# Kernel tuning notes

Hardware: AMD Instinct MI355X
Metric: run time of the kernel (lower is better)

## Reference

```python
import jax, jax.numpy as jnp
import numpy as np
import math

HID = 128
NH = 8
HD = HID // NH
NL = 3
CLIP = 10.0
EPS = 1e-5

def _ln(x, g, b):
    mu = jnp.mean(x, axis=-1, keepdims=True)
    var = jnp.var(x, axis=-1, keepdims=True)
    return (x - mu) * jax.lax.rsqrt(var + EPS) * g + b

def _layer(h, e_bias1, e_gate2, g1, b1, wh, g2, b2, w1, w2):
    B, N, _ = h.shape
    h_in = h
    hn = _ln(h, g1, b1)
    qkv = hn @ wh                                   # (B,N,3H)
    q, k, v = jnp.split(qkv, 3, axis=-1)
    q = q.reshape(B, N, NH, HD).transpose(0, 2, 1, 3)  # (B,nh,N,hd)
    k = k.reshape(B, N, NH, HD).transpose(0, 2, 1, 3)
    v = v.reshape(B, N, NH, HD).transpose(0, 2, 1, 3)
    att = jnp.einsum('bhid,bhjd->bhij', q, k) * (1.0 / math.sqrt(HD))
    att = jax.nn.softmax(att + e_bias1, axis=-1) * e_gate2
    y = jnp.einsum('bhij,bhjd->bhid', att, v)
    y = y.transpose(0, 2, 1, 3).reshape(B, N, HID)
    z = _ln(y + h_in, g2, b2)
    mlp = jax.nn.relu(z @ w1) @ w2
    return mlp + y

def setup_inputs() -> dict:
    key = jax.random.key(0)
    ks = jax.random.split(key, 9)
    d = {
        'node_features': jax.random.normal(ks[0], (16, 256, 2), jnp.float32),
        'edge_features': jax.random.normal(ks[1], (16, 256, 256, 1), jnp.float32),
        'Wn': jax.random.normal(ks[2], (2, HID), jnp.float32) * 0.5,
        'We_in': jax.random.normal(ks[3], (1, HID), jnp.float32) * 0.1,
        'ln1_g': jnp.ones((NL, HID), jnp.float32),
        'ln1_b': jnp.zeros((NL, HID), jnp.float32),
        'Wh': jax.random.normal(ks[4], (NL, HID, 3 * HID), jnp.float32) * (1.0 / math.sqrt(HID)),
        'We': jax.random.normal(ks[5], (NL, HID, 2 * NH), jnp.float32) * (1.0 / math.sqrt(HID)),
        'ln2_g': jnp.ones((NL, HID), jnp.float32),
        'ln2_b': jnp.zeros((NL, HID), jnp.float32),
        'W1': jax.random.normal(ks[6], (NL, HID, 4 * HID), jnp.float32) * (1.0 / math.sqrt(HID)),
        'W2': jax.random.normal(ks[7], (NL, 4 * HID, HID), jnp.float32) * (1.0 / math.sqrt(4 * HID)),
        'Wdec': jax.random.normal(ks[8], (HID, 1), jnp.float32) * (1.0 / math.sqrt(HID)),
    }
    return d

def reference(node_features, edge_features, Wn, We_in, ln1_g, ln1_b, Wh, We, ln2_g, ln2_b, W1, W2, Wdec):
    h = node_features @ Wn                              # (B,N,H)
    e = edge_features @ We_in                           # (B,N,N,H)
    for i in range(NL):
        ee = e @ We[i]                                  # (B,N,N,2*nh)
        ee = ee.transpose(0, 3, 1, 2)                   # (B,2*nh,N,N)
        e1, e2 = ee[:, :NH], ee[:, NH:]
        h = _layer(h, e1, e2, ln1_g[i], ln1_b[i], Wh[i], ln2_g[i], ln2_b[i], W1[i], W2[i])
    out = h @ Wdec                                      # (B,N,1)
    out = CLIP * jnp.tanh(out / math.sqrt(HID))
    return out
```

## Files before the change

### kernel.cpp

```cpp
#include <hip/hip_runtime.h>
#include <math.h>

#define HID 128
#define NHEAD 8
#define NL 3
#define NS 256
#define ROWS 4096

typedef __attribute__((ext_vector_type(8))) short bf16x8;
typedef __attribute__((ext_vector_type(4))) float f32x4;

__device__ __forceinline__ float us2f(unsigned short s) { return __uint_as_float(((unsigned)s) << 16); }
__device__ __forceinline__ unsigned short f2b(float f) {
    unsigned u = __float_as_uint(f);
    return (unsigned short)((u + 0x7fff + ((u >> 16) & 1)) >> 16);
}

__global__ __launch_bounds__(256) void k_prep(
    const float* __restrict__ Wh, const float* __restrict__ W1, const float* __restrict__ W2,
    const float* __restrict__ We_in, const float* __restrict__ We,
    const float* __restrict__ nf, const float* __restrict__ Wn,
    unsigned short* __restrict__ WhH, unsigned short* __restrict__ WhL,
    unsigned short* __restrict__ W1H, unsigned short* __restrict__ W1L,
    unsigned short* __restrict__ W2H, unsigned short* __restrict__ W2L,
    float* __restrict__ sbuf, float* __restrict__ h)
{
    int b = blockIdx.x, t = threadIdx.x;
    if (b >= 529) {
        int idx = (b - 529) * 256 + t;
        int r = idx >> 7, c = idx & 127;
        h[idx] = nf[2 * r] * Wn[c] + nf[2 * r + 1] * Wn[HID + c];
        return;
    }
    if (b == 528) {
        if (t < NL * 2 * NHEAD) {
            int l = t / (2 * NHEAD), j = t % (2 * NHEAD);
            float acc = 0.f;
            for (int c = 0; c < HID; ++c)
                acc += We_in[c] * We[(long)(l * HID + c) * (2 * NHEAD) + j];
            sbuf[t] = acc;
        }
        return;
    }
    const float* S; unsigned short *OH, *OL; int K, N, kt, nt;
    if (b < 144) {
        int l = b / 48, rem = b % 48; kt = rem & 3; nt = rem >> 2; K = 128; N = 384;
        S = Wh + (long)l * 128 * 384; OH = WhH + (long)l * 384 * 128; OL = WhL + (long)l * 384 * 128;
    } else if (b < 336) {
        int b2 = b - 144; int l = b2 / 64, rem = b2 % 64; kt = rem & 3; nt = rem >> 2; K = 128; N = 512;
        S = W1 + (long)l * 128 * 512; OH = W1H + (long)l * 512 * 128; OL = W1L + (long)l * 512 * 128;
    } else {
        int b2 = b - 336; int l = b2 / 64, rem = b2 % 64; kt = rem & 15; nt = rem >> 4; K = 512; N = 128;
        S = W2 + (long)l * 512 * 128; OH = W2H + (long)l * 128 * 512; OL = W2L + (long)l * 128 * 512;
    }
    __shared__ float sm[32][33];
    int i0 = t >> 5, j = t & 31;
#pragma unroll
    for (int p = 0; p < 4; ++p) {
        int i = i0 + p * 8;
        sm[i][j] = S[(long)(kt * 32 + i) * N + nt * 32 + j];
    }
    __syncthreads();
#pragma unroll
    for (int p = 0; p < 4; ++p) {
        int n = i0 + p * 8;
        float v = sm[j][n];
        unsigned short hh = f2b(v);
        long o = (long)(nt * 32 + n) * K + kt * 32 + j;
        OH[o] = hh; OL[o] = f2b(v - us2f(hh));
    }
}

__global__ __launch_bounds__(256) void k_fgemm(
    const float* __restrict__ x, const float* __restrict__ x2,
    const float* __restrict__ g, const float* __restrict__ b,
    const unsigned short* __restrict__ WH, const unsigned short* __restrict__ WL,
    unsigned short* __restrict__ Ch, unsigned short* __restrict__ Cl,
    int Nc, int mode)
{
    __shared__ unsigned short sAh[64 * 136], sAl[64 * 136];
    __shared__ unsigned short sWh[64 * 136], sWl[64 * 136];
    int t = threadIdx.x;
    int row0 = blockIdx.y * 64, col0 = blockIdx.x * 64;

#pragma unroll
    for (int p = 0; p < 4; ++p) {
        int rr = (t >> 4) + p * 16, ck = t & 15;
        *(uint4*)&sWh[rr * 136 + ck * 8] = *(const uint4*)&WH[(long)(col0 + rr) * 128 + ck * 8];
        *(uint4*)&sWl[rr * 136 + ck * 8] = *(const uint4*)&WL[(long)(col0 + rr) * 128 + ck * 8];
    }
#pragma unroll
    for (int pass = 0; pass < 2; ++pass) {
        int row = pass * 32 + (t >> 3);
        int p = t & 7, cb = p * 16;
        float v[16];
        const float* xp = x + (long)(row0 + row) * HID + cb;
#pragma unroll
        for (int j = 0; j < 16; j += 4) *(float4*)&v[j] = *(const float4*)(xp + j);
        if (x2) {
            const float* yp = x2 + (long)(row0 + row) * HID + cb;
#pragma unroll
            for (int j = 0; j < 16; j += 4) {
                float4 r4 = *(const float4*)(yp + j);
                v[j] += r4.x; v[j+1] += r4.y; v[j+2] += r4.z; v[j+3] += r4.w;
            }
        }
        float s = 0.f, s2 = 0.f;
#pragma unroll
        for (int j = 0; j < 16; ++j) { s += v[j]; s2 += v[j] * v[j]; }
        s  += __shfl_xor(s, 1);  s  += __shfl_xor(s, 2);  s  += __shfl_xor(s, 4);
        s2 += __shfl_xor(s2, 1); s2 += __shfl_xor(s2, 2); s2 += __shfl_xor(s2, 4);
        float mu  = s * (1.f / HID);
        float var = s2 * (1.f / HID) - mu * mu;
        float inv = rsqrtf(var + 1e-5f);
        unsigned short hi[16], lo[16];
#pragma unroll
        for (int j = 0; j < 16; ++j) {
            int c = cb + j;
            float o = (v[j] - mu) * inv * g[c] + b[c];
            hi[j] = f2b(o); lo[j] = f2b(o - us2f(hi[j]));
        }
        *(uint4*)&sAh[row * 136 + cb]     = *(uint4*)&hi[0];
        *(uint4*)&sAh[row * 136 + cb + 8] = *(uint4*)&hi[8];
        *(uint4*)&sAl[row * 136 + cb]     = *(uint4*)&lo[0];
        *(uint4*)&sAl[row * 136 + cb + 8] = *(uint4*)&lo[8];
    }
    __syncthreads();

    int w = t >> 6, lane = t & 63;
    int m = lane & 15, quad = lane >> 4;
    f32x4 acc[4];
#pragma unroll
    for (int i = 0; i < 4; ++i) acc[i] = (f32x4){0.f, 0.f, 0.f, 0.f};
#pragma unroll
    for (int c = 0; c < 4; ++c) {
        bf16x8 ah = *(const bf16x8*)&sAh[(w * 16 + m) * 136 + c * 32 + quad * 8];
        bf16x8 al = *(const bf16x8*)&sAl[(w * 16 + m) * 136 + c * 32 + quad * 8];
#pragma unroll
        for (int nt = 0; nt < 4; ++nt) {
            bf16x8 wh = *(const bf16x8*)&sWh[(nt * 16 + m) * 136 + c * 32 + quad * 8];
            bf16x8 wl = *(const bf16x8*)&sWl[(nt * 16 + m) * 136 + c * 32 + quad * 8];
            acc[nt] = __builtin_amdgcn_mfma_f32_16x16x32_bf16(ah, wh, acc[nt], 0, 0, 0);
            acc[nt] = __builtin_amdgcn_mfma_f32_16x16x32_bf16(ah, wl, acc[nt], 0, 0, 0);
            acc[nt] = __builtin_amdgcn_mfma_f32_16x16x32_bf16(al, wh, acc[nt], 0, 0, 0);
        }
    }
#pragma unroll
    for (int nt = 0; nt < 4; ++nt) {
#pragma unroll
        for (int r = 0; r < 4; ++r) {
            int row = row0 + w * 16 + quad * 4 + r;
            int col = col0 + nt * 16 + m;
            float v = acc[nt][r];
            if (mode) v = fmaxf(v, 0.f);
            unsigned short hh = f2b(v);
            Ch[(long)row * Nc + col] = hh;
            Cl[(long)row * Nc + col] = f2b(v - us2f(hh));
        }
    }
}

__global__ __launch_bounds__(256, 1) void k_mlp(
    const float* __restrict__ y, const float* __restrict__ h,
    const float* __restrict__ g, const float* __restrict__ b,
    const unsigned short* __restrict__ W1H_, const unsigned short* __restrict__ W1L_,
    const unsigned short* __restrict__ W2H_, const unsigned short* __restrict__ W2L_,
    float* __restrict__ hout, const float* __restrict__ Wdec, float* __restrict__ out)
{
    __shared__ __align__(16) unsigned short sAh[16 * 136], sAl[16 * 136];
    __shared__ __align__(16) unsigned short sHh[16 * 520], sHl[16 * 520];
    int t = threadIdx.x;
    int row0 = blockIdx.x * 16;

    if (t < 128) {
        int row = t >> 3, p = t & 7, cb = p * 16;
        float v[16];
        const float* xp = y + (long)(row0 + row) * HID + cb;
        const float* hp = h + (long)(row0 + row) * HID + cb;
#pragma unroll
        for (int j = 0; j < 16; j += 4) {
            float4 a4 = *(const float4*)(xp + j);
            float4 b4 = *(const float4*)(hp + j);
            v[j] = a4.x + b4.x; v[j+1] = a4.y + b4.y; v[j+2] = a4.z + b4.z; v[j+3] = a4.w + b4.w;
        }
        float s = 0.f, s2 = 0.f;
#pragma unroll
        for (int j = 0; j < 16; ++j) { s += v[j]; s2 += v[j] * v[j]; }
        s  += __shfl_xor(s, 1);  s  += __shfl_xor(s, 2);  s  += __shfl_xor(s, 4);
        s2 += __shfl_xor(s2, 1); s2 += __shfl_xor(s2, 2); s2 += __shfl_xor(s2, 4);
        float mu  = s * (1.f / HID);
        float var = s2 * (1.f / HID) - mu * mu;
        float inv = rsqrtf(var + 1e-5f);
        unsigned short hi[16], lo[16];
#pragma unroll
        for (int j = 0; j < 16; ++j) {
            int c = cb + j;
            float o = (v[j] - mu) * inv * g[c] + b[c];
            hi[j] = f2b(o); lo[j] = f2b(o - us2f(hi[j]));
        }
        *(uint4*)&sAh[row * 136 + cb]     = *(uint4*)&hi[0];
        *(uint4*)&sAh[row * 136 + cb + 8] = *(uint4*)&hi[8];
        *(uint4*)&sAl[row * 136 + cb]     = *(uint4*)&lo[0];
        *(uint4*)&sAl[row * 136 + cb + 8] = *(uint4*)&lo[8];
    }
    __syncthreads();

    int w = t >> 6, lane = t & 63;
    int m = lane & 15, quad = lane >> 4;

    f32x4 acc1[8];
#pragma unroll
    for (int i = 0; i < 8; ++i) acc1[i] = (f32x4){0.f, 0.f, 0.f, 0.f};
    const unsigned short* w1h = W1H_ + (long)(w * 128 + m) * 128 + quad * 8;
    const unsigned short* w1l = W1L_ + (long)(w * 128 + m) * 128 + quad * 8;
#pragma unroll
    for (int c = 0; c < 4; ++c) {
        bf16x8 ah = *(const bf16x8*)&sAh[m * 136 + c * 32 + quad * 8];
        bf16x8 al = *(const bf16x8*)&sAl[m * 136 + c * 32 + quad * 8];
#pragma unroll
        for (int nt = 0; nt < 8; ++nt) {
            bf16x8 wh = *(const bf16x8*)&w1h[nt * 16 * 128 + c * 32];
            bf16x8 wl = *(const bf16x8*)&w1l[nt * 16 * 128 + c * 32];
            acc1[nt] = __builtin_amdgcn_mfma_f32_16x16x32_bf16(wh, ah, acc1[nt], 0, 0, 0);
            acc1[nt] = __builtin_amdgcn_mfma_f32_16x16x32_bf16(wh, al, acc1[nt], 0, 0, 0);
            acc1[nt] = __builtin_amdgcn_mfma_f32_16x16x32_bf16(wl, ah, acc1[nt], 0, 0, 0);
        }
    }
#pragma unroll
    for (int nt = 0; nt < 8; ++nt) {
        unsigned short hi4[4], lo4[4];
#pragma unroll
        for (int r = 0; r < 4; ++r) {
            float v = fmaxf(acc1[nt][r], 0.f);
            hi4[r] = f2b(v);
            lo4[r] = f2b(v - us2f(hi4[r]));
        }
        int kk = w * 128 + nt * 16 + quad * 4;
        *(uint2*)&sHh[m * 520 + kk] = *(const uint2*)hi4;
        *(uint2*)&sHl[m * 520 + kk] = *(const uint2*)lo4;
    }
    __syncthreads();

    f32x4 acc2[2];
    acc2[0] = (f32x4){0.f, 0.f, 0.f, 0.f};
    acc2[1] = (f32x4){0.f, 0.f, 0.f, 0.f};
    const unsigned short* w2h = W2H_ + (long)(w * 32 + m) * 512 + quad * 8;
    const unsigned short* w2l = W2L_ + (long)(w * 32 + m) * 512 + quad * 8;
#pragma unroll
    for (int c = 0; c < 16; ++c) {
        bf16x8 ah = *(const bf16x8*)&sHh[m * 520 + c * 32 + quad * 8];
        bf16x8 al = *(const bf16x8*)&sHl[m * 520 + c * 32 + quad * 8];
#pragma unroll
        for (int nt = 0; nt < 2; ++nt) {
            bf16x8 wh = *(const bf16x8*)&w2h[nt * 16 * 512 + c * 32];
            bf16x8 wl = *(const bf16x8*)&w2l[nt * 16 * 512 + c * 32];
            acc2[nt] = __builtin_amdgcn_mfma_f32_16x16x32_bf16(ah, wh, acc2[nt], 0, 0, 0);
            acc2[nt] = __builtin_amdgcn_mfma_f32_16x16x32_bf16(ah, wl, acc2[nt], 0, 0, 0);
            acc2[nt] = __builtin_amdgcn_mfma_f32_16x16x32_bf16(al, wh, acc2[nt], 0, 0, 0);
        }
    }
    __syncthreads();
    float* ht = (float*)&sHh[0];
#pragma unroll
    for (int nt = 0; nt < 2; ++nt) {
#pragma unroll
        for (int r = 0; r < 4; ++r) {
            int row = quad * 4 + r;
            int col = w * 32 + nt * 16 + m;
            float v = acc2[nt][r] + y[(long)(row0 + row) * HID + col];
            hout[(long)(row0 + row) * HID + col] = v;
            ht[row * 132 + col] = v;
        }
    }
    if (Wdec) {
        __syncthreads();
        int row = t >> 4, sub = t & 15;
        float vv[8];
        *(float4*)&vv[0] = *(const float4*)&ht[row * 132 + sub * 8];
        *(float4*)&vv[4] = *(const float4*)&ht[row * 132 + sub * 8 + 4];
        float a = 0.f;
#pragma unroll
        for (int j = 0; j < 8; ++j) a += vv[j] * Wdec[sub * 8 + j];
        a += __shfl_xor(a, 1); a += __shfl_xor(a, 2); a += __shfl_xor(a, 4); a += __shfl_xor(a, 8);
        if (sub == 0) out[row0 + row] = 10.f * tanhf(a * 0.08838834764831845f);
    }
}

#define PAS 268
#define KQS 20
__global__ __launch_bounds__(256) void k_attn(
    const unsigned short* __restrict__ qkvH, const unsigned short* __restrict__ qkvL,
    const float* __restrict__ ef, const float* __restrict__ sbuf,
    int layer, float* __restrict__ y)
{
    __shared__ unsigned short Kh[NS * KQS], Kl[NS * KQS];
    __shared__ unsigned short Qh[64 * KQS], Ql[64 * KQS];
    __shared__ unsigned short Vh[16 * PAS], Vl[16 * PAS];
    __shared__ unsigned short Pa[4][16 * PAS];
    int bid = blockIdx.x;
    int q4 = bid & 3, hh = (bid >> 2) & 7, bb = bid >> 5;
    int t = threadIdx.x;
    {
        long kb = ((long)(bb * NS + t)) * 384 + HID + hh * 16;
        union { uint4 u[2]; unsigned short s[16]; } KH, KL, VH, VL;
        KH.u[0] = *(const uint4*)&qkvH[kb];       KH.u[1] = *(const uint4*)&qkvH[kb + 8];
        KL.u[0] = *(const uint4*)&qkvL[kb];       KL.u[1] = *(const uint4*)&qkvL[kb + 8];
        VH.u[0] = *(const uint4*)&qkvH[kb + 128]; VH.u[1] = *(const uint4*)&qkvH[kb + 136];
        VL.u[0] = *(const uint4*)&qkvL[kb + 128]; VL.u[1] = *(const uint4*)&qkvL[kb + 136];
#pragma unroll
        for (int d = 0; d < 16; ++d) {
            Kh[t * KQS + d] = KH.s[d];
            Kl[t * KQS + d] = KL.s[d];
            Vh[d * PAS + t] = VH.s[d];
            Vl[d * PAS + t] = VL.s[d];
        }
    }
    {
        int row = t >> 2, c4 = (t & 3) * 4;
        long qb = ((long)(bb * NS + q4 * 64 + row)) * 384 + hh * 16 + c4;
        union { uint2 u; unsigned short s[4]; } QH, QL;
        QH.u = *(const uint2*)&qkvH[qb];
        QL.u = *(const uint2*)&qkvL[qb];
#pragma unroll
        for (int j = 0; j < 4; ++j) {
            Qh[row * KQS + c4 + j] = QH.s[j];
            Ql[row * KQS + c4 + j] = QL.s[j];
        }
    }
    __syncthreads();
    int w = t >> 6, lane = t & 63;
    int m = lane & 15, quad = lane >> 4;
    float s1  = sbuf[layer * 16 + hh];
    float s2g = sbuf[layer * 16 + NHEAD + hh];
    unsigned short* Paw = Pa[w];

    bf16x8 qh = (bf16x8){0,0,0,0,0,0,0,0}, ql = qh;
    if (quad < 2) {
        qh = *(const bf16x8*)&Qh[(w * 16 + m) * KQS + quad * 8];
        ql = *(const bf16x8*)&Ql[(w * 16 + m) * KQS + quad * 8];
    }
    f32x4 sc[16];
#pragma unroll
    for (int ct = 0; ct < 16; ++ct) {
        bf16x8 kh = (bf16x8){0,0,0,0,0,0,0,0}, kl = kh;
        if (quad < 2) {
            kh = *(const bf16x8*)&Kh[(ct * 16 + m) * KQS + quad * 8];
            kl = *(const bf16x8*)&Kl[(ct * 16 + m) * KQS + quad * 8];
        }
        f32x4 a = (f32x4){0.f, 0.f, 0.f, 0.f};
        a = __builtin_amdgcn_mfma_f32_16x16x32_bf16(qh, kh, a, 0, 0, 0);
        a = __builtin_amdgcn_mfma_f32_16x16x32_bf16(qh, kl, a, 0, 0, 0);
        a = __builtin_amdgcn_mfma_f32_16x16x32_bf16(ql, kh, a, 0, 0, 0);
        sc[ct] = a;
    }
    int baserow = q4 * 64 + w * 16 + quad * 4;
    float s[4] = {0.f, 0.f, 0.f, 0.f};
#pragma unroll
    for (int ct = 0; ct < 16; ++ct) {
#pragma unroll
        for (int r = 0; r < 4; ++r) {
            float e = ef[((long)(bb * NS + baserow + r)) * NS + ct * 16 + m];
            float p = __expf(sc[ct][r] * 0.25f + e * s1);
            s[r] += p;
            Paw[(quad * 4 + r) * PAS + ct * 16 + m] = f2b(p * e);
        }
    }
    float inv[4];
#pragma unroll
    for (int r = 0; r < 4; ++r) {
        float ss = s[r];
        ss += __shfl_xor(ss, 1); ss += __shfl_xor(ss, 2);
        ss += __shfl_xor(ss, 4); ss += __shfl_xor(ss, 8);
        inv[r] = s2g / ss;
    }
    __syncthreads();
    f32x4 acc = (f32x4){0.f, 0.f, 0.f, 0.f};
#pragma unroll
    for (int sft = 0; sft < 8; ++sft) {
        bf16x8 pf = *(const bf16x8*)&Paw[m * PAS + sft * 32 + quad * 8];
        bf16x8 vh = *(const bf16x8*)&Vh[m * PAS + sft * 32 + quad * 8];
        bf16x8 vl = *(const bf16x8*)&Vl[m * PAS + sft * 32 + quad * 8];
        acc = __builtin_amdgcn_mfma_f32_16x16x32_bf16(pf, vh, acc, 0, 0, 0);
        acc = __builtin_amdgcn_mfma_f32_16x16x32_bf16(pf, vl, acc, 0, 0, 0);
    }
#pragma unroll
    for (int r = 0; r < 4; ++r) {
        int row = q4 * 64 + w * 16 + quad * 4 + r;
        y[((long)(bb * NS + row)) * HID + hh * 16 + m] = acc[r] * inv[r];
    }
}

extern "C" void kernel_launch(void* const* d_in, const int* in_sizes, int n_in,
                              void* d_out, int out_size, void* d_ws, size_t ws_size,
                              hipStream_t stream) {
    const float* nf    = (const float*)d_in[0];
    const float* ef    = (const float*)d_in[1];
    const float* Wn    = (const float*)d_in[2];
    const float* We_in = (const float*)d_in[3];
    const float* ln1g  = (const float*)d_in[4];
    const float* ln1b  = (const float*)d_in[5];
    const float* Wh    = (const float*)d_in[6];
    const float* We    = (const float*)d_in[7];
    const float* ln2g  = (const float*)d_in[8];
    const float* ln2b  = (const float*)d_in[9];
    const float* W1    = (const float*)d_in[10];
    const float* W2    = (const float*)d_in[11];
    const float* Wdec  = (const float*)d_in[12];

    float* ws   = (float*)d_ws;
    float* sbuf = ws;
    float* h    = ws + 64;
    float* y    = h + ROWS * HID;
    unsigned short* qkvH = (unsigned short*)(y + ROWS * HID);
    unsigned short* qkvL = qkvH + (long)ROWS * 384;
    unsigned short* WhH  = qkvL + (long)ROWS * 384;
    unsigned short* WhL  = WhH + (long)NL * 384 * 128;
    unsigned short* W1H  = WhL + (long)NL * 384 * 128;
    unsigned short* W1L  = W1H + (long)NL * 512 * 128;
    unsigned short* W2H  = W1L + (long)NL * 512 * 128;
    unsigned short* W2L  = W2H + (long)NL * 128 * 512;

    k_prep<<<529 + ROWS * HID / 256, 256, 0, stream>>>(Wh, W1, W2, We_in, We, nf, Wn,
                                    WhH, WhL, W1H, W1L, W2H, W2L, sbuf, h);
    for (int l = 0; l < NL; ++l) {
        k_fgemm<<<dim3(6, 64), 256, 0, stream>>>(h, nullptr,
            ln1g + l * HID, ln1b + l * HID,
            WhH + (long)l * 384 * 128, WhL + (long)l * 384 * 128,
            qkvH, qkvL, 384, 0);
        k_attn<<<512, 256, 0, stream>>>(qkvH, qkvL, ef, sbuf, l, y);
        int last = (l == NL - 1);
        k_mlp<<<ROWS / 16, 256, 0, stream>>>(y, h,
            ln2g + l * HID, ln2b + l * HID,
            W1H + (long)l * 512 * 128, W1L + (long)l * 512 * 128,
            W2H + (long)l * 128 * 512, W2L + (long)l * 128 * 512,
            h, last ? Wdec : nullptr, (float*)d_out);
    }
}
```

Baseline: 213.7 us.

## Widen MLP kernel to 512 threads and prefetch first weight fragments

The fused LN+MLP kernel now runs 8 wavefronts per 16-row block instead of 4, so each wave computes half as many output tiles in both GEMMs. The LayerNorm prologue is spread over all 512 threads with a 32-lane reduction. The first K-chunk of W1 and W2 fragments is loaded into registers before the barriers so global-load latency overlaps the LN and the hidden-layer store. This adds more waves to hide latency but raises per-block thread count and barrier cost.

```diff
diff --git a/kernel.cpp b/kernel.cpp
--- a/kernel.cpp
+++ b/kernel.cpp
@@ -160,7 +160,7 @@
     }
 }
 
-__global__ __launch_bounds__(256, 1) void k_mlp(
+__global__ __launch_bounds__(512, 1) void k_mlp(
     const float* __restrict__ y, const float* __restrict__ h,
     const float* __restrict__ g, const float* __restrict__ b,
     const unsigned short* __restrict__ W1H_, const unsigned short* __restrict__ W1L_,
@@ -171,63 +171,62 @@
     __shared__ __align__(16) unsigned short sHh[16 * 520], sHl[16 * 520];
     int t = threadIdx.x;
     int row0 = blockIdx.x * 16;
-
-    if (t < 128) {
-        int row = t >> 3, p = t & 7, cb = p * 16;
-        float v[16];
-        const float* xp = y + (long)(row0 + row) * HID + cb;
-        const float* hp = h + (long)(row0 + row) * HID + cb;
-#pragma unroll
-        for (int j = 0; j < 16; j += 4) {
-            float4 a4 = *(const float4*)(xp + j);
-            float4 b4 = *(const float4*)(hp + j);
-            v[j] = a4.x + b4.x; v[j+1] = a4.y + b4.y; v[j+2] = a4.z + b4.z; v[j+3] = a4.w + b4.w;
-        }
-        float s = 0.f, s2 = 0.f;
-#pragma unroll
-        for (int j = 0; j < 16; ++j) { s += v[j]; s2 += v[j] * v[j]; }
+    int w = t >> 6, lane = t & 63;
+    int m = lane & 15, quad = lane >> 4;
+
+    const unsigned short* w1h = W1H_ + (long)(w * 64 + m) * 128 + quad * 8;
+    const unsigned short* w1l = W1L_ + (long)(w * 64 + m) * 128 + quad * 8;
+    bf16x8 p1h[4], p1l[4];
+#pragma unroll
+    for (int nt = 0; nt < 4; ++nt) {
+        p1h[nt] = *(const bf16x8*)&w1h[nt * 16 * 128];
+        p1l[nt] = *(const bf16x8*)&w1l[nt * 16 * 128];
+    }
+
+    {
+        int row = t >> 5, cb = (t & 31) * 4;
+        float4 a4 = *(const float4*)&y[(long)(row0 + row) * HID + cb];
+        float4 b4 = *(const float4*)&h[(long)(row0 + row) * HID + cb];
+        float v[4] = {a4.x + b4.x, a4.y + b4.y, a4.z + b4.z, a4.w + b4.w};
+        float s = v[0] + v[1] + v[2] + v[3];
+        float s2 = v[0]*v[0] + v[1]*v[1] + v[2]*v[2] + v[3]*v[3];
         s  += __shfl_xor(s, 1);  s  += __shfl_xor(s, 2);  s  += __shfl_xor(s, 4);
+        s  += __shfl_xor(s, 8);  s  += __shfl_xor(s, 16);
         s2 += __shfl_xor(s2, 1); s2 += __shfl_xor(s2, 2); s2 += __shfl_xor(s2, 4);
+        s2 += __shfl_xor(s2, 8); s2 += __shfl_xor(s2, 16);
         float mu  = s * (1.f / HID);
         float var = s2 * (1.f / HID) - mu * mu;
         float inv = rsqrtf(var + 1e-5f);
-        unsigned short hi[16], lo[16];
-#pragma unroll
-        for (int j = 0; j < 16; ++j) {
+        unsigned short hi4[4], lo4[4];
+#pragma unroll
+        for (int j = 0; j < 4; ++j) {
             int c = cb + j;
             float o = (v[j] - mu) * inv * g[c] + b[c];
-            hi[j] = f2b(o); lo[j] = f2b(o - us2f(hi[j]));
-        }
-        *(uint4*)&sAh[row * 136 + cb]     = *(uint4*)&hi[0];
-        *(uint4*)&sAh[row * 136 + cb + 8] = *(uint4*)&hi[8];
-        *(uint4*)&sAl[row * 136 + cb]     = *(uint4*)&lo[0];
-        *(uint4*)&sAl[row * 136 + cb + 8] = *(uint4*)&lo[8];
-    }
-    __syncthreads();
-
-    int w = t >> 6, lane = t & 63;
-    int m = lane & 15, quad = lane >> 4;
-
-    f32x4 acc1[8];
-#pragma unroll
-    for (int i = 0; i < 8; ++i) acc1[i] = (f32x4){0.f, 0.f, 0.f, 0.f};
-    const unsigned short* w1h = W1H_ + (long)(w * 128 + m) * 128 + quad * 8;
-    const unsigned short* w1l = W1L_ + (long)(w * 128 + m) * 128 + quad * 8;
+            hi4[j] = f2b(o); lo4[j] = f2b(o - us2f(hi4[j]));
+        }
+        *(uint2*)&sAh[row * 136 + cb] = *(const uint2*)hi4;
+        *(uint2*)&sAl[row * 136 + cb] = *(const uint2*)lo4;
+    }
+    __syncthreads();
+
+    f32x4 acc1[4];
+#pragma unroll
+    for (int i = 0; i < 4; ++i) acc1[i] = (f32x4){0.f, 0.f, 0.f, 0.f};
 #pragma unroll
     for (int c = 0; c < 4; ++c) {
         bf16x8 ah = *(const bf16x8*)&sAh[m * 136 + c * 32 + quad * 8];
         bf16x8 al = *(const bf16x8*)&sAl[m * 136 + c * 32 + quad * 8];
 #pragma unroll
-        for (int nt = 0; nt < 8; ++nt) {
-            bf16x8 wh = *(const bf16x8*)&w1h[nt * 16 * 128 + c * 32];
-            bf16x8 wl = *(const bf16x8*)&w1l[nt * 16 * 128 + c * 32];
+        for (int nt = 0; nt < 4; ++nt) {
+            bf16x8 wh = (c == 0) ? p1h[nt] : *(const bf16x8*)&w1h[nt * 16 * 128 + c * 32];
+            bf16x8 wl = (c == 0) ? p1l[nt] : *(const bf16x8*)&w1l[nt * 16 * 128 + c * 32];
             acc1[nt] = __builtin_amdgcn_mfma_f32_16x16x32_bf16(wh, ah, acc1[nt], 0, 0, 0);
             acc1[nt] = __builtin_amdgcn_mfma_f32_16x16x32_bf16(wh, al, acc1[nt], 0, 0, 0);
             acc1[nt] = __builtin_amdgcn_mfma_f32_16x16x32_bf16(wl, ah, acc1[nt], 0, 0, 0);
         }
     }
 #pragma unroll
-    for (int nt = 0; nt < 8; ++nt) {
+    for (int nt = 0; nt < 4; ++nt) {
         unsigned short hi4[4], lo4[4];
 #pragma unroll
         for (int r = 0; r < 4; ++r) {
@@ -235,45 +234,40 @@
             hi4[r] = f2b(v);
             lo4[r] = f2b(v - us2f(hi4[r]));
         }
-        int kk = w * 128 + nt * 16 + quad * 4;
+        int kk = w * 64 + nt * 16 + quad * 4;
         *(uint2*)&sHh[m * 520 + kk] = *(const uint2*)hi4;
         *(uint2*)&sHl[m * 520 + kk] = *(const uint2*)lo4;
     }
-    __syncthreads();
-
-    f32x4 acc2[2];
-    acc2[0] = (f32x4){0.f, 0.f, 0.f, 0.f};
-    acc2[1] = (f32x4){0.f, 0.f, 0.f, 0.f};
-    const unsigned short* w2h = W2H_ + (long)(w * 32 + m) * 512 + quad * 8;
-    const unsigned short* w2l = W2L_ + (long)(w * 32 + m) * 512 + quad * 8;
+
+    const unsigned short* w2h = W2H_ + (long)(w * 16 + m) * 512 + quad * 8;
+    const unsigned short* w2l = W2L_ + (long)(w * 16 + m) * 512 + quad * 8;
+    bf16x8 p2h = *(const bf16x8*)w2h;
+    bf16x8 p2l = *(const bf16x8*)w2l;
+    __syncthreads();
+
+    f32x4 acc2 = (f32x4){0.f, 0.f, 0.f, 0.f};
 #pragma unroll
     for (int c = 0; c < 16; ++c) {
         bf16x8 ah = *(const bf16x8*)&sHh[m * 520 + c * 32 + quad * 8];
         bf16x8 al = *(const bf16x8*)&sHl[m * 520 + c * 32 + quad * 8];
-#pragma unroll
-        for (int nt = 0; nt < 2; ++nt) {
-            bf16x8 wh = *(const bf16x8*)&w2h[nt * 16 * 512 + c * 32];
-            bf16x8 wl = *(const bf16x8*)&w2l[nt * 16 * 512 + c * 32];
-            acc2[nt] = __builtin_amdgcn_mfma_f32_16x16x32_bf16(ah, wh, acc2[nt], 0, 0, 0);
-            acc2[nt] = __builtin_amdgcn_mfma_f32_16x16x32_bf16(ah, wl, acc2[nt], 0, 0, 0);
-            acc2[nt] = __builtin_amdgcn_mfma_f32_16x16x32_bf16(al, wh, acc2[nt], 0, 0, 0);
-        }
+        bf16x8 wh = (c == 0) ? p2h : *(const bf16x8*)&w2h[c * 32];
+        bf16x8 wl = (c == 0) ? p2l : *(const bf16x8*)&w2l[c * 32];
+        acc2 = __builtin_amdgcn_mfma_f32_16x16x32_bf16(ah, wh, acc2, 0, 0, 0);
+        acc2 = __builtin_amdgcn_mfma_f32_16x16x32_bf16(ah, wl, acc2, 0, 0, 0);
+        acc2 = __builtin_amdgcn_mfma_f32_16x16x32_bf16(al, wh, acc2, 0, 0, 0);
     }
     __syncthreads();
     float* ht = (float*)&sHh[0];
 #pragma unroll
-    for (int nt = 0; nt < 2; ++nt) {
-#pragma unroll
-        for (int r = 0; r < 4; ++r) {
-            int row = quad * 4 + r;
-            int col = w * 32 + nt * 16 + m;
-            float v = acc2[nt][r] + y[(long)(row0 + row) * HID + col];
-            hout[(long)(row0 + row) * HID + col] = v;
-            ht[row * 132 + col] = v;
-        }
-    }
-    if (Wdec) {
-        __syncthreads();
+    for (int r = 0; r < 4; ++r) {
+        int row = quad * 4 + r;
+        int col = w * 16 + m;
+        float v = acc2[r] + y[(long)(row0 + row) * HID + col];
+        hout[(long)(row0 + row) * HID + col] = v;
+        ht[row * 132 + col] = v;
+    }
+    __syncthreads();
+    if (Wdec && t < 256) {
         int row = t >> 4, sub = t & 15;
         float vv[8];
         *(float4*)&vv[0] = *(const float4*)&ht[row * 132 + sub * 8];
@@ -429,7 +423,7 @@
             qkvH, qkvL, 384, 0);
         k_attn<<<512, 256, 0, stream>>>(qkvH, qkvL, ef, sbuf, l, y);
         int last = (l == NL - 1);
-        k_mlp<<<ROWS / 16, 256, 0, stream>>>(y, h,
+        k_mlp<<<ROWS / 16, 512, 0, stream>>>(y, h,
             ln2g + l * HID, ln2b + l * HID,
             W1H + (long)l * 512 * 128, W1L + (long)l * 512 * 128,
             W2H + (long)l * 128 * 512, W2L + (long)l * 128 * 512,
```

New measurement: 208.0 us. -2.6%, faster.
